# Optimization experiments

Measured on AMD Instinct MI355X. Metric: run time of the kernel, lower is better.

The kernel has to match this reference:

```python
import jax, jax.numpy as jnp
import numpy as np

B, N, F = 1024, 784, 1
C1, C2, H, NCLS = 32, 32, 512, 10


def setup_inputs() -> dict:
    key = jax.random.key(0)
    ks = jax.random.split(key, 10)
    x = jax.random.normal(ks[0], (B, N, F), jnp.float32)
    # dense (renormalized-style) adjacency, shared across the batch; rows roughly sum to ~1
    a = jax.random.uniform(ks[1], (N, N), jnp.float32) * (2.0 / N)
    def glorot(k, shape):
        lim = np.sqrt(6.0 / (shape[0] + shape[1])).astype(np.float32)
        return jax.random.uniform(k, shape, jnp.float32, -lim, lim)
    return {
        "x": x,
        "a": a,
        "w1": glorot(ks[2], (F, C1)),
        "b1": jnp.zeros((C1,), jnp.float32),
        "w2": glorot(ks[3], (C1, C2)),
        "b2": jnp.zeros((C2,), jnp.float32),
        "wf1": glorot(ks[4], (N * C2, H)),
        "bf1": jnp.zeros((H,), jnp.float32),
        "wf2": glorot(ks[5], (H, NCLS)),
        "bf2": jnp.zeros((NCLS,), jnp.float32),
    }


def _graph_conv(x, a, w, b):
    # Spektral GraphConv (batch mode): elu(A @ (X @ W) + b)
    xw = jnp.einsum('bnf,fc->bnc', x, w)
    agg = jnp.einsum('nm,bmc->bnc', a, xw)
    return jax.nn.elu(agg + b)


def reference(x, a, w1, b1, w2, b2, wf1, bf1, wf2, bf2):
    h = _graph_conv(x, a, w1, b1)          # [B, N, 32]
    h = _graph_conv(h, a, w2, b2)          # [B, N, 32]
    h = h.reshape(h.shape[0], -1)          # Flatten -> [B, N*32]
    h = jax.nn.relu(h @ wf1 + bf1)         # [B, 512]
    return jax.nn.softmax(h @ wf2 + bf2, axis=-1)  # [B, 10]
```

## Files before the change

### kernel.cpp

```cpp
#include <hip/hip_runtime.h>
#include <hip/hip_bf16.h>
#include <math.h>

#define BATCH 1024
#define NREAL 784
#define NPAD  896
#define C1D   32
#define C2D   32
#define HDIM  512
#define NCLS  10
#define KFC   25088

#define KS_G1 7
#define KS_FC 14

#define BM 128
#define BN 128
#define BK 32

using bf16x8  = __attribute__((ext_vector_type(8))) __bf16;
using floatx4 = __attribute__((ext_vector_type(4))) float;

__device__ __forceinline__ float elu_f(float t) {
    return t > 0.f ? t : (__expf(t) - 1.f);
}

__device__ __forceinline__ void wg_barrier_lds() {
    asm volatile("s_waitcnt lgkmcnt(0)\n\ts_barrier" ::: "memory");
}

__device__ __forceinline__ void bar() {
    asm volatile("s_barrier" ::: "memory");
}

__device__ __forceinline__ void gload_lds16(const __hip_bfloat16* g, __hip_bfloat16* l) {
    __builtin_amdgcn_global_load_lds(
        (const __attribute__((address_space(1))) void*)g,
        (__attribute__((address_space(3))) void*)l, 16, 0, 0);
}

template<int MODE>
__launch_bounds__(256)
__global__ void gemm_bt(const __hip_bfloat16* __restrict__ A, int lda,
                        const __hip_bfloat16* __restrict__ Bm, int ldb,
                        int kIters, int kPerZ, size_t sliceStride,
                        float* __restrict__ outF, int ldc,
                        __hip_bfloat16* __restrict__ outH,
                        const float* __restrict__ bias)
{
    __shared__ __align__(16) __hip_bfloat16 As[2][BM * BK];
    __shared__ __align__(16) __hip_bfloat16 Bs[2][BN * BK];

    const int tid  = threadIdx.x;
    const int lane = tid & 63;
    const int wave = tid >> 6;
    const int wi = wave >> 1, wj = wave & 1;

    const int m0 = blockIdx.y * BM;
    const int n0 = blockIdx.x * BN;
    const int kBase = blockIdx.z * kPerZ;

    const int rowInChunk = lane >> 2;
    const int kOff8 = (lane & 3) * 8;

    const __hip_bfloat16* aSrc0 = A  + (size_t)(m0 + (wave * 2 + 0) * 16 + rowInChunk) * lda + kBase + kOff8;
    const __hip_bfloat16* aSrc1 = A  + (size_t)(m0 + (wave * 2 + 1) * 16 + rowInChunk) * lda + kBase + kOff8;
    const __hip_bfloat16* bSrc0 = Bm + (size_t)(n0 + (wave * 2 + 0) * 16 + rowInChunk) * ldb + kBase + kOff8;
    const __hip_bfloat16* bSrc1 = Bm + (size_t)(n0 + (wave * 2 + 1) * 16 + rowInChunk) * ldb + kBase + kOff8;

    const int wSlot = (((lane & 3) + ((lane >> 3) & 3)) & 3) * 8;
    const int ldsW0 = (wave * 2 + 0) * 512 + rowInChunk * 32 + wSlot;
    const int ldsW1 = ldsW0 + 512;

    const int rSlot = ((((lane >> 4) + (((lane & 15) >> 1) & 3)) & 3)) * 8;
    const int rRow  = lane & 15;

    floatx4 acc[4][4];
    const floatx4 zero4 = {0.f, 0.f, 0.f, 0.f};
    #pragma unroll
    for (int i = 0; i < 4; i++)
        #pragma unroll
        for (int j = 0; j < 4; j++) acc[i][j] = zero4;

    int4 aA0, aA1, bA0, bA1;
    int4 aB0, aB1, bB0, bB1;

    aA0 = *(const int4*)aSrc0; aA1 = *(const int4*)aSrc1;
    bA0 = *(const int4*)bSrc0; bA1 = *(const int4*)bSrc1;
    aSrc0 += BK; aSrc1 += BK; bSrc0 += BK; bSrc1 += BK;
    aB0 = *(const int4*)aSrc0; aB1 = *(const int4*)aSrc1;
    bB0 = *(const int4*)bSrc0; bB1 = *(const int4*)bSrc1;
    aSrc0 += BK; aSrc1 += BK; bSrc0 += BK; bSrc1 += BK;

    *(int4*)(&As[0][ldsW0]) = aA0;
    *(int4*)(&As[0][ldsW1]) = aA1;
    *(int4*)(&Bs[0][ldsW0]) = bA0;
    *(int4*)(&Bs[0][ldsW1]) = bA1;
    wg_barrier_lds();

    for (int kt = 0; kt < kIters; kt += 2) {
        const bool more = (kt + 2 < kIters);

        {
            bf16x8 af[4], bfr[4];
            #pragma unroll
            for (int mi = 0; mi < 4; mi++)
                af[mi] = *(const bf16x8*)(&As[0][(wi * 64 + mi * 16 + rRow) * BK + rSlot]);
            #pragma unroll
            for (int nj = 0; nj < 4; nj++)
                bfr[nj] = *(const bf16x8*)(&Bs[0][(wj * 64 + nj * 16 + rRow) * BK + rSlot]);

            if (more) {
                aA0 = *(const int4*)aSrc0; aA1 = *(const int4*)aSrc1;
                bA0 = *(const int4*)bSrc0; bA1 = *(const int4*)bSrc1;
                aSrc0 += BK; aSrc1 += BK; bSrc0 += BK; bSrc1 += BK;
            }
            *(int4*)(&As[1][ldsW0]) = aB0;
            *(int4*)(&As[1][ldsW1]) = aB1;
            *(int4*)(&Bs[1][ldsW0]) = bB0;
            *(int4*)(&Bs[1][ldsW1]) = bB1;

            #pragma unroll
            for (int mi = 0; mi < 4; mi++)
                #pragma unroll
                for (int nj = 0; nj < 4; nj++)
                    acc[mi][nj] = __builtin_amdgcn_mfma_f32_16x16x32_bf16(af[mi], bfr[nj], acc[mi][nj], 0, 0, 0);

            wg_barrier_lds();
        }

        {
            bf16x8 af[4], bfr[4];
            #pragma unroll
            for (int mi = 0; mi < 4; mi++)
                af[mi] = *(const bf16x8*)(&As[1][(wi * 64 + mi * 16 + rRow) * BK + rSlot]);
            #pragma unroll
            for (int nj = 0; nj < 4; nj++)
                bfr[nj] = *(const bf16x8*)(&Bs[1][(wj * 64 + nj * 16 + rRow) * BK + rSlot]);

            if (more) {
                aB0 = *(const int4*)aSrc0; aB1 = *(const int4*)aSrc1;
                bB0 = *(const int4*)bSrc0; bB1 = *(const int4*)bSrc1;
                aSrc0 += BK; aSrc1 += BK; bSrc0 += BK; bSrc1 += BK;
                *(int4*)(&As[0][ldsW0]) = aA0;
                *(int4*)(&As[0][ldsW1]) = aA1;
                *(int4*)(&Bs[0][ldsW0]) = bA0;
                *(int4*)(&Bs[0][ldsW1]) = bA1;
            }

            #pragma unroll
            for (int mi = 0; mi < 4; mi++)
                #pragma unroll
                for (int nj = 0; nj < 4; nj++)
                    acc[mi][nj] = __builtin_amdgcn_mfma_f32_16x16x32_bf16(af[mi], bfr[nj], acc[mi][nj], 0, 0, 0);

            wg_barrier_lds();
        }
    }

    #pragma unroll
    for (int mi = 0; mi < 4; mi++) {
        #pragma unroll
        for (int nj = 0; nj < 4; nj++) {
            #pragma unroll
            for (int r = 0; r < 4; r++) {
                const int row = m0 + wi * 64 + mi * 16 + (lane >> 4) * 4 + r;
                const int col = n0 + wj * 64 + nj * 16 + (lane & 15);
                const float v = acc[mi][nj][r];
                if (MODE == 1) {
                    if (row < NREAL) {
                        const int c = col & 31, b = col >> 5;
                        const float t = elu_f(v + bias[c]);
                        outH[(size_t)b * KFC + row * 32 + c] = __float2bfloat16(t);
                    }
                } else {
                    outF[(size_t)blockIdx.z * sliceStride + (size_t)row * ldc + col] = v;
                }
            }
        }
    }
}

#define KT_G3 14

#define STAGE_A(tt, hh) do {                                                    \
    const int s_ = (2 * (tt) + (hh)) & 3;                                       \
    gload_lds16(aSrcH[hh][0] + (tt) * 64, &Ah[s_][(wave * 2 + 0) * 512]);       \
    gload_lds16(aSrcH[hh][1] + (tt) * 64, &Ah[s_][(wave * 2 + 1) * 512]);       \
} while (0)

#define STAGE_B(tt, hh) do {                                                    \
    const int s_ = (2 * (tt) + (hh)) & 3;                                       \
    gload_lds16(bSrcH[hh][0] + (tt) * 64, &Bh[s_][(wave * 2 + 0) * 512]);       \
    gload_lds16(bSrcH[hh][1] + (tt) * 64, &Bh[s_][(wave * 2 + 1) * 512]);       \
} while (0)

__launch_bounds__(512, 2)
__global__ void gemm256_g3(const __hip_bfloat16* __restrict__ Ag,
                           const __hip_bfloat16* __restrict__ Bg,
                           __hip_bfloat16* __restrict__ outH,
                           const float* __restrict__ bias)
{
    __shared__ __align__(16) __hip_bfloat16 Ah[4][128 * 64];
    __shared__ __align__(16) __hip_bfloat16 Bh[4][128 * 64];

    const int tid  = threadIdx.x;
    const int lane = tid & 63;
    const int wave = tid >> 6;
    const int vm = wave >> 2, vn = wave & 3;

    const int mR = blockIdx.y * 256;
    const int nR = blockIdx.x * 256;

    const int rRow = lane & 15;
    const int gHi  = lane >> 4;
    const int rot  = lane & 7;
    const int koff0 = (((gHi + rot) & 7) << 3);
    const int koff1 = ((((gHi + 4) + rot) & 7) << 3);
    const int aBase = (vm * 64 + rRow) * 64;
    const int bBase = (vn * 32 + rRow) * 64;

    const int rowLoc = lane >> 3;
    const int gOff   = ((((lane & 7) - rowLoc) & 7) << 3);
    const __hip_bfloat16* aSrcH[2][2];
    const __hip_bfloat16* bSrcH[2][2];
    #pragma unroll
    for (int h = 0; h < 2; h++)
        #pragma unroll
        for (int j = 0; j < 2; j++) {
            int ra = mR + h * 128 + (wave * 2 + j) * 8 + rowLoc;
            if (ra > NPAD - 1) ra = NPAD - 1;
            aSrcH[h][j] = Ag + (size_t)ra * NPAD + gOff;
            const int rb = nR + h * 128 + (wave * 2 + j) * 8 + rowLoc;
            bSrcH[h][j] = Bg + (size_t)rb * NPAD + gOff;
        }

    const float bias0 = bias[rRow];
    const float bias1 = bias[16 + rRow];

    floatx4 acc[4][4][2];
    const floatx4 zero4 = {0.f, 0.f, 0.f, 0.f};
    #pragma unroll
    for (int q = 0; q < 4; q++)
        #pragma unroll
        for (int i = 0; i < 4; i++)
            #pragma unroll
            for (int j = 0; j < 2; j++) acc[q][i][j] = zero4;

    STAGE_A(0, 0); STAGE_B(0, 1);
    STAGE_A(0, 1); STAGE_B(0, 0);
    STAGE_A(1, 0); STAGE_B(1, 1);

    #pragma unroll 2
    for (int t = 0; t < KT_G3; ++t) {
        if (t + 1 < KT_G3) { asm volatile("s_waitcnt vmcnt(4)" ::: "memory"); }
        else               { asm volatile("s_waitcnt vmcnt(0)" ::: "memory"); }
        bar();

        const int sA0 = (2 * t + 0) & 3, sA1 = (2 * t + 1) & 3;
        const int sB0 = (2 * t + 0) & 3, sB1 = (2 * t + 1) & 3;

        bf16x8 aF[4][2], bF[2][2];

        #pragma unroll
        for (int mi = 0; mi < 4; mi++) {
            aF[mi][0] = *(const bf16x8*)(&Ah[sA0][aBase + mi * 1024 + koff0]);
            aF[mi][1] = *(const bf16x8*)(&Ah[sA0][aBase + mi * 1024 + koff1]);
        }
        #pragma unroll
        for (int nj = 0; nj < 2; nj++) {
            bF[nj][0] = *(const bf16x8*)(&Bh[sB0][bBase + nj * 1024 + koff0]);
            bF[nj][1] = *(const bf16x8*)(&Bh[sB0][bBase + nj * 1024 + koff1]);
        }
        if (t + 1 < KT_G3) { STAGE_A(t + 1, 1); STAGE_B(t + 1, 0); }
        __builtin_amdgcn_s_setprio(1);
        #pragma unroll
        for (int mi = 0; mi < 4; mi++)
            #pragma unroll
            for (int nj = 0; nj < 2; nj++)
                acc[0][mi][nj] = __builtin_amdgcn_mfma_f32_16x16x32_bf16(aF[mi][0], bF[nj][0], acc[0][mi][nj], 0, 0, 0);
        #pragma unroll
        for (int mi = 0; mi < 4; mi++)
            #pragma unroll
            for (int nj = 0; nj < 2; nj++)
                acc[0][mi][nj] = __builtin_amdgcn_mfma_f32_16x16x32_bf16(aF[mi][1], bF[nj][1], acc[0][mi][nj], 0, 0, 0);
        __builtin_amdgcn_s_setprio(0);

        #pragma unroll
        for (int nj = 0; nj < 2; nj++) {
            bF[nj][0] = *(const bf16x8*)(&Bh[sB1][bBase + nj * 1024 + koff0]);
            bF[nj][1] = *(const bf16x8*)(&Bh[sB1][bBase + nj * 1024 + koff1]);
        }
        __builtin_amdgcn_s_setprio(1);
        #pragma unroll
        for (int mi = 0; mi < 4; mi++)
            #pragma unroll
            for (int nj = 0; nj < 2; nj++)
                acc[1][mi][nj] = __builtin_amdgcn_mfma_f32_16x16x32_bf16(aF[mi][0], bF[nj][0], acc[1][mi][nj], 0, 0, 0);
        #pragma unroll
        for (int mi = 0; mi < 4; mi++)
            #pragma unroll
            for (int nj = 0; nj < 2; nj++)
                acc[1][mi][nj] = __builtin_amdgcn_mfma_f32_16x16x32_bf16(aF[mi][1], bF[nj][1], acc[1][mi][nj], 0, 0, 0);
        __builtin_amdgcn_s_setprio(0);

        bar();

        #pragma unroll
        for (int mi = 0; mi < 4; mi++) {
            aF[mi][0] = *(const bf16x8*)(&Ah[sA1][aBase + mi * 1024 + koff0]);
            aF[mi][1] = *(const bf16x8*)(&Ah[sA1][aBase + mi * 1024 + koff1]);
        }
        if (t + 2 < KT_G3) { STAGE_A(t + 2, 0); STAGE_B(t + 2, 1); }
        __builtin_amdgcn_s_setprio(1);
        #pragma unroll
        for (int mi = 0; mi < 4; mi++)
            #pragma unroll
            for (int nj = 0; nj < 2; nj++)
                acc[3][mi][nj] = __builtin_amdgcn_mfma_f32_16x16x32_bf16(aF[mi][0], bF[nj][0], acc[3][mi][nj], 0, 0, 0);
        #pragma unroll
        for (int mi = 0; mi < 4; mi++)
            #pragma unroll
            for (int nj = 0; nj < 2; nj++)
                acc[3][mi][nj] = __builtin_amdgcn_mfma_f32_16x16x32_bf16(aF[mi][1], bF[nj][1], acc[3][mi][nj], 0, 0, 0);
        __builtin_amdgcn_s_setprio(0);

        #pragma unroll
        for (int nj = 0; nj < 2; nj++) {
            bF[nj][0] = *(const bf16x8*)(&Bh[sB0][bBase + nj * 1024 + koff0]);
            bF[nj][1] = *(const bf16x8*)(&Bh[sB0][bBase + nj * 1024 + koff1]);
        }
        __builtin_amdgcn_s_setprio(1);
        #pragma unroll
        for (int mi = 0; mi < 4; mi++)
            #pragma unroll
            for (int nj = 0; nj < 2; nj++)
                acc[2][mi][nj] = __builtin_amdgcn_mfma_f32_16x16x32_bf16(aF[mi][0], bF[nj][0], acc[2][mi][nj], 0, 0, 0);
        #pragma unroll
        for (int mi = 0; mi < 4; mi++)
            #pragma unroll
            for (int nj = 0; nj < 2; nj++)
                acc[2][mi][nj] = __builtin_amdgcn_mfma_f32_16x16x32_bf16(aF[mi][1], bF[nj][1], acc[2][mi][nj], 0, 0, 0);
        __builtin_amdgcn_s_setprio(0);
    }

    #pragma unroll
    for (int q = 0; q < 4; q++) {
        const int qm = q >> 1, qn = q & 1;
        #pragma unroll
        for (int mi = 0; mi < 4; mi++) {
            #pragma unroll
            for (int nj = 0; nj < 2; nj++) {
                #pragma unroll
                for (int r = 0; r < 4; r++) {
                    const int row = mR + qm * 128 + vm * 64 + mi * 16 + gHi * 4 + r;
                    if (row < NREAL) {
                        const int col = nR + qn * 128 + vn * 32 + nj * 16 + rRow;
                        const int c = col & 31, b = col >> 5;
                        const float bv = nj ? bias1 : bias0;
                        const float v = elu_f(acc[q][mi][nj][r] + bv);
                        outH[(size_t)b * KFC + row * 32 + c] = __float2bfloat16(v);
                    }
                }
            }
        }
    }
}

__global__ void convX(const float* __restrict__ x, __hip_bfloat16* __restrict__ Xbf) {
    const int idx = blockIdx.x * 256 + threadIdx.x;
    if (idx >= BATCH * NPAD) return;
    const int m = idx % NPAD, b = idx / NPAD;
    const float v = (m < NREAL) ? x[(size_t)b * NREAL + m] : 0.f;
    Xbf[idx] = __float2bfloat16(v);
}

__global__ void convA(const float* __restrict__ a, __hip_bfloat16* __restrict__ Abf) {
    const int idx = blockIdx.x * 256 + threadIdx.x;
    if (idx >= NPAD * NPAD) return;
    const int m = idx % NPAD, n = idx / NPAD;
    const float v = (m < NREAL && n < NREAL) ? a[(size_t)n * NREAL + m] : 0.f;
    Abf[idx] = __float2bfloat16(v);
}

__global__ void convW(const float* __restrict__ wf1, __hip_bfloat16* __restrict__ Wt) {
    __shared__ float tile[32][33];
    const int k0 = blockIdx.x * 32, h0 = blockIdx.y * 32;
    const int tx = threadIdx.x, ty = threadIdx.y;
    #pragma unroll
    for (int i = 0; i < 4; i++)
        tile[ty * 4 + i][tx] = wf1[(size_t)(k0 + ty * 4 + i) * HDIM + h0 + tx];
    __syncthreads();
    #pragma unroll
    for (int i = 0; i < 4; i++)
        Wt[(size_t)(h0 + ty * 4 + i) * KFC + k0 + tx] = __float2bfloat16(tile[tx][ty * 4 + i]);
}

__global__ void layer1_fuse(const float* __restrict__ Ypart,
                            const float* __restrict__ w1, const float* __restrict__ b1,
                            const float* __restrict__ w2,
                            __hip_bfloat16* __restrict__ Tt)
{
    __shared__ __align__(16) float sW2[C1D * C2D];
    __shared__ float sw1[C1D], sb1[C1D];
    const int tid = threadIdx.x;
    for (int i = tid; i < C1D * C2D; i += 128) sW2[i] = w2[i];
    if (tid < C1D) { sw1[tid] = w1[tid]; sb1[tid] = b1[tid]; }
    __syncthreads();

    const int m = blockIdx.x * 128 + tid;
    const int b = blockIdx.y;
    float y = 0.f;
    #pragma unroll
    for (int z = 0; z < KS_G1; z++)
        y += Ypart[(size_t)z * (BATCH * NPAD) + (size_t)b * NPAD + m];

    float h[C1D];
    #pragma unroll
    for (int c1 = 0; c1 < C1D; c1++) h[c1] = elu_f(y * sw1[c1] + sb1[c1]);

    float4 t4[8];
    #pragma unroll
    for (int q = 0; q < 8; q++) t4[q] = make_float4(0.f, 0.f, 0.f, 0.f);
    #pragma unroll
    for (int c1 = 0; c1 < C1D; c1++) {
        const float hv = h[c1];
        const float4* row = (const float4*)(sW2 + c1 * C2D);
        #pragma unroll
        for (int q = 0; q < 8; q++) {
            const float4 w = row[q];
            t4[q].x += hv * w.x; t4[q].y += hv * w.y;
            t4[q].z += hv * w.z; t4[q].w += hv * w.w;
        }
    }
    const float* tf = (const float*)t4;
    #pragma unroll
    for (int c = 0; c < C2D; c++)
        Tt[((size_t)(b * 32 + c)) * NPAD + m] = __float2bfloat16(tf[c]);
}

__global__ void fc2_softmax(const float* __restrict__ part, const float* __restrict__ bf1,
                            const float* __restrict__ wf2, const float* __restrict__ bf2,
                            float* __restrict__ out)
{
    __shared__ float sW[HDIM * NCLS];
    __shared__ float sb[NCLS];
    const int tid = threadIdx.x;
    for (int i = tid; i < HDIM * NCLS; i += 256) sW[i] = wf2[i];
    if (tid < NCLS) sb[tid] = bf2[tid];
    __syncthreads();

    const int lane = tid & 63, wave = tid >> 6;
    const int b = blockIdx.x * 4 + wave;

    float acc[NCLS];
    #pragma unroll
    for (int c = 0; c < NCLS; c++) acc[c] = 0.f;
    #pragma unroll
    for (int q = 0; q < 8; q++) {
        const int h = q * 64 + lane;
        float hv = bf1[h];
        #pragma unroll
        for (int z = 0; z < KS_FC; z++)
            hv += part[(size_t)z * (BATCH * HDIM) + (size_t)b * HDIM + h];
        hv = hv > 0.f ? hv : 0.f;
        #pragma unroll
        for (int c = 0; c < NCLS; c++) acc[c] += hv * sW[h * NCLS + c];
    }
    #pragma unroll
    for (int c = 0; c < NCLS; c++) {
        #pragma unroll
        for (int off = 32; off >= 1; off >>= 1) acc[c] += __shfl_down(acc[c], off);
    }
    if (lane == 0) {
        float mx = -1e30f;
        #pragma unroll
        for (int c = 0; c < NCLS; c++) { acc[c] += sb[c]; mx = fmaxf(mx, acc[c]); }
        float e[NCLS], s = 0.f;
        #pragma unroll
        for (int c = 0; c < NCLS; c++) { e[c] = __expf(acc[c] - mx); s += e[c]; }
        const float inv = 1.f / s;
        #pragma unroll
        for (int c = 0; c < NCLS; c++) out[(size_t)b * NCLS + c] = e[c] * inv;
    }
}

extern "C" void kernel_launch(void* const* d_in, const int* in_sizes, int n_in,
                              void* d_out, int out_size, void* d_ws, size_t ws_size,
                              hipStream_t stream)
{
    const float* x   = (const float*)d_in[0];
    const float* a   = (const float*)d_in[1];
    const float* w1  = (const float*)d_in[2];
    const float* b1  = (const float*)d_in[3];
    const float* w2  = (const float*)d_in[4];
    const float* b2  = (const float*)d_in[5];
    const float* wf1 = (const float*)d_in[6];
    const float* bf1 = (const float*)d_in[7];
    const float* wf2 = (const float*)d_in[8];
    const float* bf2 = (const float*)d_in[9];
    float* out = (float*)d_out;

    char* ws = (char*)d_ws;
    __hip_bfloat16* h2f  = (__hip_bfloat16*)(ws + 0);
    float*          Ypart= (float*)(ws + 0);
    __hip_bfloat16* Tt   = (__hip_bfloat16*)(ws + 51380224);
    __hip_bfloat16* Wt   = (__hip_bfloat16*)(ws + 51380224);
    float*          part = (float*)(ws + 77070336);
    __hip_bfloat16* Abf  = (__hip_bfloat16*)(ws + 110100480);
    __hip_bfloat16* Xbf  = (__hip_bfloat16*)(ws + 111706112);

    convX<<<(BATCH * NPAD + 255) / 256, 256, 0, stream>>>(x, Xbf);
    convA<<<(NPAD * NPAD + 255) / 256, 256, 0, stream>>>(a, Abf);

    gemm_bt<2><<<dim3(NPAD / BN, BATCH / BM, KS_G1), 256, 0, stream>>>(
        Xbf, NPAD, Abf, NPAD, (NPAD / KS_G1) / BK, NPAD / KS_G1,
        (size_t)BATCH * NPAD, Ypart, NPAD, nullptr, nullptr);

    layer1_fuse<<<dim3(NPAD / 128, BATCH), 128, 0, stream>>>(Ypart, w1, b1, w2, Tt);

    gemm256_g3<<<dim3(BATCH * 32 / 256, 1024 / 256), 512, 0, stream>>>(Abf, Tt, h2f, b2);

    convW<<<dim3(KFC / 32, HDIM / 32), dim3(32, 8), 0, stream>>>(wf1, Wt);

    gemm_bt<2><<<dim3(HDIM / BN, BATCH / BM, KS_FC), 256, 0, stream>>>(
        h2f, KFC, Wt, KFC, (KFC / KS_FC) / BK, KFC / KS_FC,
        (size_t)BATCH * HDIM, part, HDIM, nullptr, nullptr);

    fc2_softmax<<<BATCH / 4, 256, 0, stream>>>(part, bf1, wf2, bf2, out);
}
```

Before: 273.3 us.

## Replace register-staged GEMM with direct-to-LDS 4-stage pipelined 128x128 kernel

Swaps the generic split-K GEMM, which staged tiles through registers into LDS with BK=32 double buffering, for a new kernel. The new kernel loads global memory straight into LDS with global_load_lds over a 4-slot ring, uses BK=64 tiles with a rotated swizzle, and raises MFMA priority. It also splits the reused B-fragment registers in gemm256_g3 into two sets so one LDS reload is dropped, and merges the X and A conversion kernels into one launch. The aim is less VGPR staging, fewer barriers per K step and more load/compute overlap, at the cost of more LDS per block (64 KB) and a full vmcnt wait at every step.

```diff
diff --git a/kernel.cpp b/kernel.cpp
--- a/kernel.cpp
+++ b/kernel.cpp
@@ -14,19 +14,11 @@
 #define KS_G1 7
 #define KS_FC 14
 
-#define BM 128
-#define BN 128
-#define BK 32
-
 using bf16x8  = __attribute__((ext_vector_type(8))) __bf16;
 using floatx4 = __attribute__((ext_vector_type(4))) float;
 
 __device__ __forceinline__ float elu_f(float t) {
     return t > 0.f ? t : (__expf(t) - 1.f);
-}
-
-__device__ __forceinline__ void wg_barrier_lds() {
-    asm volatile("s_waitcnt lgkmcnt(0)\n\ts_barrier" ::: "memory");
 }
 
 __device__ __forceinline__ void bar() {
@@ -39,41 +31,55 @@
         (__attribute__((address_space(3))) void*)l, 16, 0, 0);
 }
 
-template<int MODE>
-__launch_bounds__(256)
-__global__ void gemm_bt(const __hip_bfloat16* __restrict__ A, int lda,
-                        const __hip_bfloat16* __restrict__ Bm, int ldb,
-                        int kIters, int kPerZ, size_t sliceStride,
-                        float* __restrict__ outF, int ldc,
-                        __hip_bfloat16* __restrict__ outH,
-                        const float* __restrict__ bias)
-{
-    __shared__ __align__(16) __hip_bfloat16 As[2][BM * BK];
-    __shared__ __align__(16) __hip_bfloat16 Bs[2][BN * BK];
+#define STAGE128_A(tt, hh) do {                                                 \
+    const int s_ = (2 * (tt) + (hh)) & 3;                                       \
+    gload_lds16(aSrcH[hh][0] + (tt) * 64, &Ah[s_][(wave * 2 + 0) * 512]);       \
+    gload_lds16(aSrcH[hh][1] + (tt) * 64, &Ah[s_][(wave * 2 + 1) * 512]);       \
+} while (0)
+
+#define STAGE128_B(tt, hh) do {                                                 \
+    const int s_ = (2 * (tt) + (hh)) & 3;                                       \
+    gload_lds16(bSrcH[hh][0] + (tt) * 64, &Bh[s_][(wave * 2 + 0) * 512]);       \
+    gload_lds16(bSrcH[hh][1] + (tt) * 64, &Bh[s_][(wave * 2 + 1) * 512]);       \
+} while (0)
+
+__launch_bounds__(256, 2)
+__global__ void gemm128_rg(const __hip_bfloat16* __restrict__ A, int lda,
+                           const __hip_bfloat16* __restrict__ Bm, int ldb,
+                           int kTiles, int kPerZ, size_t sliceStride,
+                           float* __restrict__ outF, int ldc)
+{
+    __shared__ __align__(16) __hip_bfloat16 Ah[4][64 * 64];
+    __shared__ __align__(16) __hip_bfloat16 Bh[4][64 * 64];
 
     const int tid  = threadIdx.x;
     const int lane = tid & 63;
     const int wave = tid >> 6;
-    const int wi = wave >> 1, wj = wave & 1;
-
-    const int m0 = blockIdx.y * BM;
-    const int n0 = blockIdx.x * BN;
+    const int vm = wave >> 1, vn = wave & 1;
+
+    const int m0 = blockIdx.y * 128;
+    const int n0 = blockIdx.x * 128;
     const int kBase = blockIdx.z * kPerZ;
 
-    const int rowInChunk = lane >> 2;
-    const int kOff8 = (lane & 3) * 8;
-
-    const __hip_bfloat16* aSrc0 = A  + (size_t)(m0 + (wave * 2 + 0) * 16 + rowInChunk) * lda + kBase + kOff8;
-    const __hip_bfloat16* aSrc1 = A  + (size_t)(m0 + (wave * 2 + 1) * 16 + rowInChunk) * lda + kBase + kOff8;
-    const __hip_bfloat16* bSrc0 = Bm + (size_t)(n0 + (wave * 2 + 0) * 16 + rowInChunk) * ldb + kBase + kOff8;
-    const __hip_bfloat16* bSrc1 = Bm + (size_t)(n0 + (wave * 2 + 1) * 16 + rowInChunk) * ldb + kBase + kOff8;
-
-    const int wSlot = (((lane & 3) + ((lane >> 3) & 3)) & 3) * 8;
-    const int ldsW0 = (wave * 2 + 0) * 512 + rowInChunk * 32 + wSlot;
-    const int ldsW1 = ldsW0 + 512;
-
-    const int rSlot = ((((lane >> 4) + (((lane & 15) >> 1) & 3)) & 3)) * 8;
-    const int rRow  = lane & 15;
+    const int rRow = lane & 15;
+    const int gHi  = lane >> 4;
+    const int rot  = lane & 7;
+    const int koff0 = (((gHi + rot) & 7) << 3);
+    const int koff1 = ((((gHi + 4) + rot) & 7) << 3);
+
+    const int rowLoc = lane >> 3;
+    const int gOff   = ((((lane & 7) - rowLoc) & 7) << 3);
+    const __hip_bfloat16* aSrcH[2][2];
+    const __hip_bfloat16* bSrcH[2][2];
+    #pragma unroll
+    for (int h = 0; h < 2; h++)
+        #pragma unroll
+        for (int j = 0; j < 2; j++) {
+            const int ra = m0 + h * 64 + (wave * 2 + j) * 8 + rowLoc;
+            aSrcH[h][j] = A  + (size_t)ra * lda + kBase + gOff;
+            const int rb = n0 + h * 64 + (wave * 2 + j) * 8 + rowLoc;
+            bSrcH[h][j] = Bm + (size_t)rb * ldb + kBase + gOff;
+        }
 
     floatx4 acc[4][4];
     const floatx4 zero4 = {0.f, 0.f, 0.f, 0.f};
@@ -82,80 +88,48 @@
         #pragma unroll
         for (int j = 0; j < 4; j++) acc[i][j] = zero4;
 
-    int4 aA0, aA1, bA0, bA1;
-    int4 aB0, aB1, bB0, bB1;
-
-    aA0 = *(const int4*)aSrc0; aA1 = *(const int4*)aSrc1;
-    bA0 = *(const int4*)bSrc0; bA1 = *(const int4*)bSrc1;
-    aSrc0 += BK; aSrc1 += BK; bSrc0 += BK; bSrc1 += BK;
-    aB0 = *(const int4*)aSrc0; aB1 = *(const int4*)aSrc1;
-    bB0 = *(const int4*)bSrc0; bB1 = *(const int4*)bSrc1;
-    aSrc0 += BK; aSrc1 += BK; bSrc0 += BK; bSrc1 += BK;
-
-    *(int4*)(&As[0][ldsW0]) = aA0;
-    *(int4*)(&As[0][ldsW1]) = aA1;
-    *(int4*)(&Bs[0][ldsW0]) = bA0;
-    *(int4*)(&Bs[0][ldsW1]) = bA1;
-    wg_barrier_lds();
-
-    for (int kt = 0; kt < kIters; kt += 2) {
-        const bool more = (kt + 2 < kIters);
-
-        {
-            bf16x8 af[4], bfr[4];
-            #pragma unroll
-            for (int mi = 0; mi < 4; mi++)
-                af[mi] = *(const bf16x8*)(&As[0][(wi * 64 + mi * 16 + rRow) * BK + rSlot]);
+    STAGE128_A(0, 0); STAGE128_A(0, 1);
+    STAGE128_B(0, 0); STAGE128_B(0, 1);
+
+    #pragma unroll 2
+    for (int t = 0; t < kTiles; ++t) {
+        asm volatile("s_waitcnt vmcnt(0)" ::: "memory");
+        bar();
+
+        const int sA = (2 * t + vm) & 3;
+        const int sB = (2 * t + vn) & 3;
+        const __hip_bfloat16* Ab = &Ah[sA][rRow * 64];
+        const __hip_bfloat16* Bb = &Bh[sB][rRow * 64];
+
+        bf16x8 aF[4][2], bF[4][2];
+        #pragma unroll
+        for (int mi = 0; mi < 4; mi++) {
+            aF[mi][0] = *(const bf16x8*)(Ab + mi * 1024 + koff0);
+            aF[mi][1] = *(const bf16x8*)(Ab + mi * 1024 + koff1);
+        }
+        #pragma unroll
+        for (int nj = 0; nj < 4; nj++) {
+            bF[nj][0] = *(const bf16x8*)(Bb + nj * 1024 + koff0);
+            bF[nj][1] = *(const bf16x8*)(Bb + nj * 1024 + koff1);
+        }
+
+        if (t + 1 < kTiles) {
+            STAGE128_A(t + 1, 0); STAGE128_A(t + 1, 1);
+            STAGE128_B(t + 1, 0); STAGE128_B(t + 1, 1);
+        }
+
+        __builtin_amdgcn_s_setprio(1);
+        #pragma unroll
+        for (int mi = 0; mi < 4; mi++)
             #pragma unroll
             for (int nj = 0; nj < 4; nj++)
-                bfr[nj] = *(const bf16x8*)(&Bs[0][(wj * 64 + nj * 16 + rRow) * BK + rSlot]);
-
-            if (more) {
-                aA0 = *(const int4*)aSrc0; aA1 = *(const int4*)aSrc1;
-                bA0 = *(const int4*)bSrc0; bA1 = *(const int4*)bSrc1;
-                aSrc0 += BK; aSrc1 += BK; bSrc0 += BK; bSrc1 += BK;
-            }
-            *(int4*)(&As[1][ldsW0]) = aB0;
-            *(int4*)(&As[1][ldsW1]) = aB1;
-            *(int4*)(&Bs[1][ldsW0]) = bB0;
-            *(int4*)(&Bs[1][ldsW1]) = bB1;
-
-            #pragma unroll
-            for (int mi = 0; mi < 4; mi++)
-                #pragma unroll
-                for (int nj = 0; nj < 4; nj++)
-                    acc[mi][nj] = __builtin_amdgcn_mfma_f32_16x16x32_bf16(af[mi], bfr[nj], acc[mi][nj], 0, 0, 0);
-
-            wg_barrier_lds();
-        }
-
-        {
-            bf16x8 af[4], bfr[4];
-            #pragma unroll
-            for (int mi = 0; mi < 4; mi++)
-                af[mi] = *(const bf16x8*)(&As[1][(wi * 64 + mi * 16 + rRow) * BK + rSlot]);
+                acc[mi][nj] = __builtin_amdgcn_mfma_f32_16x16x32_bf16(aF[mi][0], bF[nj][0], acc[mi][nj], 0, 0, 0);
+        #pragma unroll
+        for (int mi = 0; mi < 4; mi++)
             #pragma unroll
             for (int nj = 0; nj < 4; nj++)
-                bfr[nj] = *(const bf16x8*)(&Bs[1][(wj * 64 + nj * 16 + rRow) * BK + rSlot]);
-
-            if (more) {
-                aB0 = *(const int4*)aSrc0; aB1 = *(const int4*)aSrc1;
-                bB0 = *(const int4*)bSrc0; bB1 = *(const int4*)bSrc1;
-                aSrc0 += BK; aSrc1 += BK; bSrc0 += BK; bSrc1 += BK;
-                *(int4*)(&As[0][ldsW0]) = aA0;
-                *(int4*)(&As[0][ldsW1]) = aA1;
-                *(int4*)(&Bs[0][ldsW0]) = bA0;
-                *(int4*)(&Bs[0][ldsW1]) = bA1;
-            }
-
-            #pragma unroll
-            for (int mi = 0; mi < 4; mi++)
-                #pragma unroll
-                for (int nj = 0; nj < 4; nj++)
-                    acc[mi][nj] = __builtin_amdgcn_mfma_f32_16x16x32_bf16(af[mi], bfr[nj], acc[mi][nj], 0, 0, 0);
-
-            wg_barrier_lds();
-        }
+                acc[mi][nj] = __builtin_amdgcn_mfma_f32_16x16x32_bf16(aF[mi][1], bF[nj][1], acc[mi][nj], 0, 0, 0);
+        __builtin_amdgcn_s_setprio(0);
     }
 
     #pragma unroll
@@ -164,18 +138,9 @@
         for (int nj = 0; nj < 4; nj++) {
             #pragma unroll
             for (int r = 0; r < 4; r++) {
-                const int row = m0 + wi * 64 + mi * 16 + (lane >> 4) * 4 + r;
-                const int col = n0 + wj * 64 + nj * 16 + (lane & 15);
-                const float v = acc[mi][nj][r];
-                if (MODE == 1) {
-                    if (row < NREAL) {
-                        const int c = col & 31, b = col >> 5;
-                        const float t = elu_f(v + bias[c]);
-                        outH[(size_t)b * KFC + row * 32 + c] = __float2bfloat16(t);
-                    }
-                } else {
-                    outF[(size_t)blockIdx.z * sliceStride + (size_t)row * ldc + col] = v;
-                }
+                const int row = m0 + vm * 64 + mi * 16 + gHi * 4 + r;
+                const int col = n0 + vn * 64 + nj * 16 + rRow;
+                outF[(size_t)blockIdx.z * sliceStride + (size_t)row * ldc + col] = acc[mi][nj][r];
             }
         }
     }
@@ -260,7 +225,7 @@
         const int sA0 = (2 * t + 0) & 3, sA1 = (2 * t + 1) & 3;
         const int sB0 = (2 * t + 0) & 3, sB1 = (2 * t + 1) & 3;
 
-        bf16x8 aF[4][2], bF[2][2];
+        bf16x8 aF[4][2], bF0[2][2], bF1[2][2];
 
         #pragma unroll
         for (int mi = 0; mi < 4; mi++) {
@@ -269,8 +234,8 @@
         }
         #pragma unroll
         for (int nj = 0; nj < 2; nj++) {
-            bF[nj][0] = *(const bf16x8*)(&Bh[sB0][bBase + nj * 1024 + koff0]);
-            bF[nj][1] = *(const bf16x8*)(&Bh[sB0][bBase + nj * 1024 + koff1]);
+            bF0[nj][0] = *(const bf16x8*)(&Bh[sB0][bBase + nj * 1024 + koff0]);
+            bF0[nj][1] = *(const bf16x8*)(&Bh[sB0][bBase + nj * 1024 + koff1]);
         }
         if (t + 1 < KT_G3) { STAGE_A(t + 1, 1); STAGE_B(t + 1, 0); }
         __builtin_amdgcn_s_setprio(1);
@@ -278,30 +243,30 @@
         for (int mi = 0; mi < 4; mi++)
             #pragma unroll
             for (int nj = 0; nj < 2; nj++)
-                acc[0][mi][nj] = __builtin_amdgcn_mfma_f32_16x16x32_bf16(aF[mi][0], bF[nj][0], acc[0][mi][nj], 0, 0, 0);
-        #pragma unroll
-        for (int mi = 0; mi < 4; mi++)
-            #pragma unroll
-            for (int nj = 0; nj < 2; nj++)
-                acc[0][mi][nj] = __builtin_amdgcn_mfma_f32_16x16x32_bf16(aF[mi][1], bF[nj][1], acc[0][mi][nj], 0, 0, 0);
+                acc[0][mi][nj] = __builtin_amdgcn_mfma_f32_16x16x32_bf16(aF[mi][0], bF0[nj][0], acc[0][mi][nj], 0, 0, 0);
+        #pragma unroll
+        for (int mi = 0; mi < 4; mi++)
+            #pragma unroll
+            for (int nj = 0; nj < 2; nj++)
+                acc[0][mi][nj] = __builtin_amdgcn_mfma_f32_16x16x32_bf16(aF[mi][1], bF0[nj][1], acc[0][mi][nj], 0, 0, 0);
         __builtin_amdgcn_s_setprio(0);
 
         #pragma unroll
         for (int nj = 0; nj < 2; nj++) {
-            bF[nj][0] = *(const bf16x8*)(&Bh[sB1][bBase + nj * 1024 + koff0]);
-            bF[nj][1] = *(const bf16x8*)(&Bh[sB1][bBase + nj * 1024 + koff1]);
+            bF1[nj][0] = *(const bf16x8*)(&Bh[sB1][bBase + nj * 1024 + koff0]);
+            bF1[nj][1] = *(const bf16x8*)(&Bh[sB1][bBase + nj * 1024 + koff1]);
         }
         __builtin_amdgcn_s_setprio(1);
         #pragma unroll
         for (int mi = 0; mi < 4; mi++)
             #pragma unroll
             for (int nj = 0; nj < 2; nj++)
-                acc[1][mi][nj] = __builtin_amdgcn_mfma_f32_16x16x32_bf16(aF[mi][0], bF[nj][0], acc[1][mi][nj], 0, 0, 0);
-        #pragma unroll
-        for (int mi = 0; mi < 4; mi++)
-            #pragma unroll
-            for (int nj = 0; nj < 2; nj++)
-                acc[1][mi][nj] = __builtin_amdgcn_mfma_f32_16x16x32_bf16(aF[mi][1], bF[nj][1], acc[1][mi][nj], 0, 0, 0);
+                acc[1][mi][nj] = __builtin_amdgcn_mfma_f32_16x16x32_bf16(aF[mi][0], bF1[nj][0], acc[1][mi][nj], 0, 0, 0);
+        #pragma unroll
+        for (int mi = 0; mi < 4; mi++)
+            #pragma unroll
+            for (int nj = 0; nj < 2; nj++)
+                acc[1][mi][nj] = __builtin_amdgcn_mfma_f32_16x16x32_bf16(aF[mi][1], bF1[nj][1], acc[1][mi][nj], 0, 0, 0);
         __builtin_amdgcn_s_setprio(0);
 
         bar();
@@ -317,30 +282,25 @@
         for (int mi = 0; mi < 4; mi++)
             #pragma unroll
             for (int nj = 0; nj < 2; nj++)
-                acc[3][mi][nj] = __builtin_amdgcn_mfma_f32_16x16x32_bf16(aF[mi][0], bF[nj][0], acc[3][mi][nj], 0, 0, 0);
-        #pragma unroll
-        for (int mi = 0; mi < 4; mi++)
-            #pragma unroll
-            for (int nj = 0; nj < 2; nj++)
-                acc[3][mi][nj] = __builtin_amdgcn_mfma_f32_16x16x32_bf16(aF[mi][1], bF[nj][1], acc[3][mi][nj], 0, 0, 0);
+                acc[3][mi][nj] = __builtin_amdgcn_mfma_f32_16x16x32_bf16(aF[mi][0], bF1[nj][0], acc[3][mi][nj], 0, 0, 0);
+        #pragma unroll
+        for (int mi = 0; mi < 4; mi++)
+            #pragma unroll
+            for (int nj = 0; nj < 2; nj++)
+                acc[3][mi][nj] = __builtin_amdgcn_mfma_f32_16x16x32_bf16(aF[mi][1], bF1[nj][1], acc[3][mi][nj], 0, 0, 0);
         __builtin_amdgcn_s_setprio(0);
 
-        #pragma unroll
-        for (int nj = 0; nj < 2; nj++) {
-            bF[nj][0] = *(const bf16x8*)(&Bh[sB0][bBase + nj * 1024 + koff0]);
-            bF[nj][1] = *(const bf16x8*)(&Bh[sB0][bBase + nj * 1024 + koff1]);
-        }
         __builtin_amdgcn_s_setprio(1);
         #pragma unroll
         for (int mi = 0; mi < 4; mi++)
             #pragma unroll
             for (int nj = 0; nj < 2; nj++)
-                acc[2][mi][nj] = __builtin_amdgcn_mfma_f32_16x16x32_bf16(aF[mi][0], bF[nj][0], acc[2][mi][nj], 0, 0, 0);
-        #pragma unroll
-        for (int mi = 0; mi < 4; mi++)
-            #pragma unroll
-            for (int nj = 0; nj < 2; nj++)
-                acc[2][mi][nj] = __builtin_amdgcn_mfma_f32_16x16x32_bf16(aF[mi][1], bF[nj][1], acc[2][mi][nj], 0, 0, 0);
+                acc[2][mi][nj] = __builtin_amdgcn_mfma_f32_16x16x32_bf16(aF[mi][0], bF0[nj][0], acc[2][mi][nj], 0, 0, 0);
+        #pragma unroll
+        for (int mi = 0; mi < 4; mi++)
+            #pragma unroll
+            for (int nj = 0; nj < 2; nj++)
+                acc[2][mi][nj] = __builtin_amdgcn_mfma_f32_16x16x32_bf16(aF[mi][1], bF0[nj][1], acc[2][mi][nj], 0, 0, 0);
         __builtin_amdgcn_s_setprio(0);
     }
 
@@ -367,20 +327,25 @@
     }
 }
 
-__global__ void convX(const float* __restrict__ x, __hip_bfloat16* __restrict__ Xbf) {
-    const int idx = blockIdx.x * 256 + threadIdx.x;
-    if (idx >= BATCH * NPAD) return;
-    const int m = idx % NPAD, b = idx / NPAD;
-    const float v = (m < NREAL) ? x[(size_t)b * NREAL + m] : 0.f;
-    Xbf[idx] = __float2bfloat16(v);
-}
-
-__global__ void convA(const float* __restrict__ a, __hip_bfloat16* __restrict__ Abf) {
-    const int idx = blockIdx.x * 256 + threadIdx.x;
-    if (idx >= NPAD * NPAD) return;
-    const int m = idx % NPAD, n = idx / NPAD;
-    const float v = (m < NREAL && n < NREAL) ? a[(size_t)n * NREAL + m] : 0.f;
-    Abf[idx] = __float2bfloat16(v);
+#define NBLK_X ((BATCH * NPAD + 255) / 256)
+#define NBLK_A ((NPAD * NPAD + 255) / 256)
+
+__global__ void convXA(const float* __restrict__ x, __hip_bfloat16* __restrict__ Xbf,
+                       const float* __restrict__ a, __hip_bfloat16* __restrict__ Abf)
+{
+    if (blockIdx.x < NBLK_X) {
+        const int idx = blockIdx.x * 256 + threadIdx.x;
+        if (idx >= BATCH * NPAD) return;
+        const int m = idx % NPAD, b = idx / NPAD;
+        const float v = (m < NREAL) ? x[(size_t)b * NREAL + m] : 0.f;
+        Xbf[idx] = __float2bfloat16(v);
+    } else {
+        const int idx = (blockIdx.x - NBLK_X) * 256 + threadIdx.x;
+        if (idx >= NPAD * NPAD) return;
+        const int m = idx % NPAD, n = idx / NPAD;
+        const float v = (m < NREAL && n < NREAL) ? a[(size_t)n * NREAL + m] : 0.f;
+        Abf[idx] = __float2bfloat16(v);
+    }
 }
 
 __global__ void convW(const float* __restrict__ wf1, __hip_bfloat16* __restrict__ Wt) {
@@ -510,12 +475,11 @@
     __hip_bfloat16* Abf  = (__hip_bfloat16*)(ws + 110100480);
     __hip_bfloat16* Xbf  = (__hip_bfloat16*)(ws + 111706112);
 
-    convX<<<(BATCH * NPAD + 255) / 256, 256, 0, stream>>>(x, Xbf);
-    convA<<<(NPAD * NPAD + 255) / 256, 256, 0, stream>>>(a, Abf);
-
-    gemm_bt<2><<<dim3(NPAD / BN, BATCH / BM, KS_G1), 256, 0, stream>>>(
-        Xbf, NPAD, Abf, NPAD, (NPAD / KS_G1) / BK, NPAD / KS_G1,
-        (size_t)BATCH * NPAD, Ypart, NPAD, nullptr, nullptr);
+    convXA<<<NBLK_X + NBLK_A, 256, 0, stream>>>(x, Xbf, a, Abf);
+
+    gemm128_rg<<<dim3(NPAD / 128, BATCH / 128, KS_G1), 256, 0, stream>>>(
+        Xbf, NPAD, Abf, NPAD, (NPAD / KS_G1) / 64, NPAD / KS_G1,
+        (size_t)BATCH * NPAD, Ypart, NPAD);
 
     layer1_fuse<<<dim3(NPAD / 128, BATCH), 128, 0, stream>>>(Ypart, w1, b1, w2, Tt);
 
@@ -523,9 +487,9 @@
 
     convW<<<dim3(KFC / 32, HDIM / 32), dim3(32, 8), 0, stream>>>(wf1, Wt);
 
-    gemm_bt<2><<<dim3(HDIM / BN, BATCH / BM, KS_FC), 256, 0, stream>>>(
-        h2f, KFC, Wt, KFC, (KFC / KS_FC) / BK, KFC / KS_FC,
-        (size_t)BATCH * HDIM, part, HDIM, nullptr, nullptr);
+    gemm128_rg<<<dim3(HDIM / 128, BATCH / 128, KS_FC), 256, 0, stream>>>(
+        h2f, KFC, Wt, KFC, (KFC / KS_FC) / 64, KFC / KS_FC,
+        (size_t)BATCH * HDIM, part, HDIM);
 
     fc2_softmax<<<BATCH / 4, 256, 0, stream>>>(part, bf1, wf2, bf2, out);
 }
```

After: 265.1 us. 3.0% less time.
